# Optimization experiments

Hardware: AMD Instinct MI355X
Metric: run time of the kernel (lower is better)

Reference implementation:

```python
import jax, jax.numpy as jnp
import numpy as np

DIV_COEF = 1.0
EPS = 1e-8  # torch.cosine_similarity default eps


def setup_inputs() -> dict:
    key = jax.random.key(0)
    id_ = jax.random.normal(key, (8192, 512), dtype=jnp.float32)
    return {"id": id_}


def reference(id):
    # cosine similarity via norm + GEMM (math identical to broadcast form)
    norms = jnp.linalg.norm(id, axis=1)                      # [N]
    dots = id @ id.T                                          # [N, N]
    sim = dots / jnp.maximum(norms[:, None] * norms[None, :], EPS)
    n = id.shape[0]
    # zero diagonal, clamp negatives to zero, mean over full NxN
    off_diag = 1.0 - jnp.eye(n, dtype=sim.dtype)
    id_sim = off_diag * sim
    l_id_div = jnp.mean(jnp.where(id_sim < 0, 0.0, id_sim))
    total_loss = DIV_COEF * l_id_div
    return (total_loss, l_id_div)
```

## Files before the change

### kernel.cpp

```cpp
#include <hip/hip_runtime.h>
#include <stdint.h>

#define NROWS 8192
#define KDIM  512
#define BM    256
#define BK    64
#define NKI   (KDIM / BK)
#define NT    (NROWS / BM)
#define NBLK  (NT * (NT + 1) / 2)

typedef __attribute__((ext_vector_type(4)))  int   i32x4;
typedef __attribute__((ext_vector_type(8)))  int   i32x8;
typedef __attribute__((ext_vector_type(16))) float f32x16;

__device__ __forceinline__ void async_copy16(const unsigned char* g, unsigned char* l) {
  __builtin_amdgcn_global_load_lds(
      (const __attribute__((address_space(1))) unsigned int*)g,
      (__attribute__((address_space(3))) unsigned int*)l,
      16, 0, 0);
}

__global__ __launch_bounds__(256) void prep_kernel(
    const float* __restrict__ src, unsigned char* __restrict__ dst,
    float* __restrict__ acc) {
  const int row  = blockIdx.x * 4 + (threadIdx.x >> 6);
  const int lane = threadIdx.x & 63;
  const float4 v0 = ((const float4*)src)[row * 128 + lane * 2];
  const float4 v1 = ((const float4*)src)[row * 128 + lane * 2 + 1];
  float ss = v0.x * v0.x + v0.y * v0.y + v0.z * v0.z + v0.w * v0.w
           + v1.x * v1.x + v1.y * v1.y + v1.z * v1.z + v1.w * v1.w;
  #pragma unroll
  for (int off = 32; off > 0; off >>= 1) ss += __shfl_down(ss, off);
  const float rn = 1.0f / sqrtf(__shfl(ss, 0));
  if (row == 0 && lane == 0) { acc[0] = 0.0f; ((unsigned int*)acc)[1] = 0u; }
  int pk0 = __builtin_amdgcn_cvt_pk_fp8_f32(v0.x * rn, v0.y * rn, 0, false);
  pk0     = __builtin_amdgcn_cvt_pk_fp8_f32(v0.z * rn, v0.w * rn, pk0, true);
  int pk1 = __builtin_amdgcn_cvt_pk_fp8_f32(v1.x * rn, v1.y * rn, 0, false);
  pk1     = __builtin_amdgcn_cvt_pk_fp8_f32(v1.z * rn, v1.w * rn, pk1, true);
  const int cg  = lane >> 1;
  const int win = cg >> 2;
  const int p   = (cg & 3) ^ ((row >> 1) & 3);
  const int hf  = lane & 1;
  uint2 o; o.x = (unsigned int)pk0; o.y = (unsigned int)pk1;
  ((uint2*)dst)[row * 64 + win * 8 + p * 2 + hf] = o;
}

__device__ __forceinline__ int tri_base(int b) {
  return b * NT - (b * (b - 1)) / 2;
}

__global__ __launch_bounds__(512, 2) void sim_reduce_kernel(
    const unsigned char* __restrict__ idn, float* __restrict__ acc,
    float* __restrict__ out) {
  const int idx = blockIdx.x;
  const float Af = 2.0f * NT + 1.0f;
  int bi = (int)((Af - sqrtf(Af * Af - 8.0f * (float)idx)) * 0.5f);
  while (bi > 0 && tri_base(bi) > idx) bi--;
  while (tri_base(bi + 1) <= idx) bi++;
  const int bj = bi + (idx - tri_base(bi));

  __shared__ __align__(16) unsigned char As[2][BM * BK];
  __shared__ __align__(16) unsigned char Bs[2][BM * BK];

  const int tid  = threadIdx.x;
  const int lane = tid & 63;
  const int w    = tid >> 6;
  const int wrow = (w >> 2) * 128;
  const int wcol = (w & 3) * 64;
  const int r32  = lane & 31;
  const int h    = lane >> 5;
  const int rx   = (r32 >> 1) & 3;

  f32x16 acc_f[4][2];
  #pragma unroll
  for (int i = 0; i < 4; i++)
    #pragma unroll
    for (int j = 0; j < 2; j++)
      acc_f[i][j] = (f32x16){0.f, 0.f, 0.f, 0.f, 0.f, 0.f, 0.f, 0.f,
                             0.f, 0.f, 0.f, 0.f, 0.f, 0.f, 0.f, 0.f};

  const unsigned char* gA = idn + (size_t)(bi * BM + (tid >> 2)) * KDIM + (tid & 3) * 16;
  const unsigned char* gB = idn + (size_t)(bj * BM + (tid >> 2)) * KDIM + (tid & 3) * 16;
  const int ldso = tid * 16;

  #pragma unroll
  for (int i = 0; i < 2; i++) async_copy16(gA + (size_t)i * 65536, &As[0][ldso + i * 8192]);
  #pragma unroll
  for (int i = 0; i < 2; i++) async_copy16(gB + (size_t)i * 65536, &Bs[0][ldso + i * 8192]);

  const int p0 = ((2 * h)     ^ rx) * 16;
  const int p1 = ((2 * h + 1) ^ rx) * 16;

  #pragma unroll
  for (int t = 0; t < NKI; ++t) {
    const int cs = t & 1;
    if (t + 1 < NKI) {
      const int ns = cs ^ 1;
      const int ko = (t + 1) * BK;
      #pragma unroll
      for (int i = 0; i < 2; i++)
        async_copy16(gA + ko + (size_t)i * 65536, &As[ns][ldso + i * 8192]);
      #pragma unroll
      for (int i = 0; i < 2; i++)
        async_copy16(gB + ko + (size_t)i * 65536, &Bs[ns][ldso + i * 8192]);
      asm volatile("s_waitcnt vmcnt(4)" ::: "memory");
    } else {
      asm volatile("s_waitcnt vmcnt(0)" ::: "memory");
    }
    asm volatile("s_barrier" ::: "memory");

    i32x8 af[4], bf[2];
    #pragma unroll
    for (int mi = 0; mi < 4; mi++) {
      const unsigned char* ab = &As[cs][(wrow + mi * 32 + r32) * BK];
      const i32x4 alo = *(const i32x4*)(ab + p0);
      const i32x4 ahi = *(const i32x4*)(ab + p1);
      af[mi] = __builtin_shufflevector(alo, ahi, 0, 1, 2, 3, 4, 5, 6, 7);
    }
    #pragma unroll
    for (int ni = 0; ni < 2; ni++) {
      const unsigned char* bb = &Bs[cs][(wcol + ni * 32 + r32) * BK];
      const i32x4 blo = *(const i32x4*)(bb + p0);
      const i32x4 bhi = *(const i32x4*)(bb + p1);
      bf[ni] = __builtin_shufflevector(blo, bhi, 0, 1, 2, 3, 4, 5, 6, 7);
    }
    #pragma unroll
    for (int mi = 0; mi < 4; mi++)
      #pragma unroll
      for (int ni = 0; ni < 2; ni++)
        acc_f[mi][ni] = __builtin_amdgcn_mfma_scale_f32_32x32x64_f8f6f4(
            af[mi], bf[ni], acc_f[mi][ni],
            0, 0,
            0, 0x7F7F7F7Fu,
            0, 0x7F7F7F7Fu);

    asm volatile("s_barrier" ::: "memory");
  }

  float local = 0.f;
  const bool diag = (bi == bj);
  #pragma unroll
  for (int mi = 0; mi < 4; mi++)
    #pragma unroll
    for (int ni = 0; ni < 2; ni++)
      #pragma unroll
      for (int rg = 0; rg < 16; rg++) {
        const int ri = wrow + mi * 32 + (rg & 3) + 8 * (rg >> 2) + 4 * h;
        const int ci = wcol + ni * 32 + r32;
        float v = fmaxf(acc_f[mi][ni][rg], 0.f);
        if (diag && ri == ci) v = 0.f;
        local += v;
      }

  #pragma unroll
  for (int off = 32; off > 0; off >>= 1) local += __shfl_down(local, off);
  __syncthreads();
  float* red = (float*)As;
  if (lane == 0) red[w] = local;
  __syncthreads();
  if (tid == 0) {
    float s = red[0] + red[1] + red[2] + red[3]
            + red[4] + red[5] + red[6] + red[7];
    if (!diag) s *= 2.f;
    atomicAdd(acc, s);
    __threadfence();
    unsigned int done = atomicAdd((unsigned int*)(acc + 1), 1u);
    if (done == NBLK - 1) {
      float total = atomicAdd(acc, 0.0f);
      const float m = total * (1.0f / ((float)NROWS * (float)NROWS));
      out[0] = m;
      out[1] = m;
    }
  }
}

extern "C" void kernel_launch(void* const* d_in, const int* in_sizes, int n_in,
                              void* d_out, int out_size, void* d_ws, size_t ws_size,
                              hipStream_t stream) {
  const float* id = (const float*)d_in[0];
  float* out = (float*)d_out;
  unsigned char* idn = (unsigned char*)d_ws;
  float* acc = (float*)((char*)d_ws + (size_t)NROWS * KDIM);

  prep_kernel<<<NROWS / 4, 256, 0, stream>>>(id, idn, acc);
  sim_reduce_kernel<<<NBLK, 512, 0, stream>>>(idn, acc, out);
}
```

Measured before the change: 96.34 us.

## Split tail triangle tiles into half-height blocks to balance the final wave

The first 512 triangular tiles keep the full 256x256 blocks. The remaining 16 tiles are each split into two 128x256 half blocks, which adds work units for the last partial wave across the CUs. MFMA sections are also wrapped in s_setprio to favour matrix issue. The half blocks reload the B tile, adding some redundant loads, and the runtime MN branch can add overhead or registers in the full path.

Result: slower. 152.8 us (+58.6%).

```diff
diff --git a/kernel.cpp b/kernel.cpp
--- a/kernel.cpp
+++ b/kernel.cpp
@@ -8,6 +8,8 @@
 #define NKI   (KDIM / BK)
 #define NT    (NROWS / BM)
 #define NBLK  (NT * (NT + 1) / 2)
+#define NFULL 512
+#define NGRID (NFULL + 2 * (NBLK - NFULL))
 
 typedef __attribute__((ext_vector_type(4)))  int   i32x4;
 typedef __attribute__((ext_vector_type(8)))  int   i32x8;
@@ -52,7 +54,12 @@
 __global__ __launch_bounds__(512, 2) void sim_reduce_kernel(
     const unsigned char* __restrict__ idn, float* __restrict__ acc,
     float* __restrict__ out) {
-  const int idx = blockIdx.x;
+  const bool fullb = ((int)blockIdx.x < NFULL);
+  const int  idx   = fullb ? (int)blockIdx.x
+                           : NFULL + (((int)blockIdx.x - NFULL) >> 1);
+  const int  half  = fullb ? 0 : (((int)blockIdx.x - NFULL) & 1);
+  const int  MN    = fullb ? 4 : 2;
+
   const float Af = 2.0f * NT + 1.0f;
   int bi = (int)((Af - sqrtf(Af * Af - 8.0f * (float)idx)) * 0.5f);
   while (bi > 0 && tri_base(bi) > idx) bi--;
@@ -65,8 +72,9 @@
   const int tid  = threadIdx.x;
   const int lane = tid & 63;
   const int w    = tid >> 6;
-  const int wrow = (w >> 2) * 128;
-  const int wcol = (w & 3) * 64;
+  const int mrows = fullb ? 128 : 64;
+  const int wrow  = (w >> 2) * mrows;
+  const int wcol  = (w & 3) * 64;
   const int r32  = lane & 31;
   const int h    = lane >> 5;
   const int rx   = (r32 >> 1) & 3;
@@ -79,12 +87,14 @@
       acc_f[i][j] = (f32x16){0.f, 0.f, 0.f, 0.f, 0.f, 0.f, 0.f, 0.f,
                              0.f, 0.f, 0.f, 0.f, 0.f, 0.f, 0.f, 0.f};
 
-  const unsigned char* gA = idn + (size_t)(bi * BM + (tid >> 2)) * KDIM + (tid & 3) * 16;
+  const unsigned char* gA =
+      idn + (size_t)(bi * BM + half * 128 + (tid >> 2)) * KDIM + (tid & 3) * 16;
   const unsigned char* gB = idn + (size_t)(bj * BM + (tid >> 2)) * KDIM + (tid & 3) * 16;
+  const size_t aStride = fullb ? 65536 : 0;
   const int ldso = tid * 16;
 
   #pragma unroll
-  for (int i = 0; i < 2; i++) async_copy16(gA + (size_t)i * 65536, &As[0][ldso + i * 8192]);
+  for (int i = 0; i < 2; i++) async_copy16(gA + (size_t)i * aStride, &As[0][ldso + i * 8192]);
   #pragma unroll
   for (int i = 0; i < 2; i++) async_copy16(gB + (size_t)i * 65536, &Bs[0][ldso + i * 8192]);
 
@@ -99,7 +109,7 @@
       const int ko = (t + 1) * BK;
       #pragma unroll
       for (int i = 0; i < 2; i++)
-        async_copy16(gA + ko + (size_t)i * 65536, &As[ns][ldso + i * 8192]);
+        async_copy16(gA + ko + (size_t)i * aStride, &As[ns][ldso + i * 8192]);
       #pragma unroll
       for (int i = 0; i < 2; i++)
         async_copy16(gB + ko + (size_t)i * 65536, &Bs[ns][ldso + i * 8192]);
@@ -111,13 +121,6 @@
 
     i32x8 af[4], bf[2];
     #pragma unroll
-    for (int mi = 0; mi < 4; mi++) {
-      const unsigned char* ab = &As[cs][(wrow + mi * 32 + r32) * BK];
-      const i32x4 alo = *(const i32x4*)(ab + p0);
-      const i32x4 ahi = *(const i32x4*)(ab + p1);
-      af[mi] = __builtin_shufflevector(alo, ahi, 0, 1, 2, 3, 4, 5, 6, 7);
-    }
-    #pragma unroll
     for (int ni = 0; ni < 2; ni++) {
       const unsigned char* bb = &Bs[cs][(wcol + ni * 32 + r32) * BK];
       const i32x4 blo = *(const i32x4*)(bb + p0);
@@ -126,31 +129,43 @@
     }
     #pragma unroll
     for (int mi = 0; mi < 4; mi++)
+      if (mi < MN) {
+        const unsigned char* ab = &As[cs][(wrow + mi * 32 + r32) * BK];
+        const i32x4 alo = *(const i32x4*)(ab + p0);
+        const i32x4 ahi = *(const i32x4*)(ab + p1);
+        af[mi] = __builtin_shufflevector(alo, ahi, 0, 1, 2, 3, 4, 5, 6, 7);
+      }
+    __builtin_amdgcn_s_setprio(1);
+    #pragma unroll
+    for (int mi = 0; mi < 4; mi++)
+      if (mi < MN)
+        #pragma unroll
+        for (int ni = 0; ni < 2; ni++)
+          acc_f[mi][ni] = __builtin_amdgcn_mfma_scale_f32_32x32x64_f8f6f4(
+              af[mi], bf[ni], acc_f[mi][ni],
+              0, 0,
+              0, 0x7F7F7F7Fu,
+              0, 0x7F7F7F7Fu);
+    __builtin_amdgcn_s_setprio(0);
+
+    asm volatile("s_barrier" ::: "memory");
+  }
+
+  float local = 0.f;
+  const bool diag = (bi == bj);
+  #pragma unroll
+  for (int mi = 0; mi < 4; mi++)
+    if (mi < MN)
       #pragma unroll
       for (int ni = 0; ni < 2; ni++)
-        acc_f[mi][ni] = __builtin_amdgcn_mfma_scale_f32_32x32x64_f8f6f4(
-            af[mi], bf[ni], acc_f[mi][ni],
-            0, 0,
-            0, 0x7F7F7F7Fu,
-            0, 0x7F7F7F7Fu);
-
-    asm volatile("s_barrier" ::: "memory");
-  }
-
-  float local = 0.f;
-  const bool diag = (bi == bj);
-  #pragma unroll
-  for (int mi = 0; mi < 4; mi++)
-    #pragma unroll
-    for (int ni = 0; ni < 2; ni++)
-      #pragma unroll
-      for (int rg = 0; rg < 16; rg++) {
-        const int ri = wrow + mi * 32 + (rg & 3) + 8 * (rg >> 2) + 4 * h;
-        const int ci = wcol + ni * 32 + r32;
-        float v = fmaxf(acc_f[mi][ni][rg], 0.f);
-        if (diag && ri == ci) v = 0.f;
-        local += v;
-      }
+        #pragma unroll
+        for (int rg = 0; rg < 16; rg++) {
+          const int ri = half * 128 + wrow + mi * 32 + (rg & 3) + 8 * (rg >> 2) + 4 * h;
+          const int ci = wcol + ni * 32 + r32;
+          float v = fmaxf(acc_f[mi][ni][rg], 0.f);
+          if (diag && ri == ci) v = 0.f;
+          local += v;
+        }
 
   #pragma unroll
   for (int off = 32; off > 0; off >>= 1) local += __shfl_down(local, off);
@@ -165,7 +180,7 @@
     atomicAdd(acc, s);
     __threadfence();
     unsigned int done = atomicAdd((unsigned int*)(acc + 1), 1u);
-    if (done == NBLK - 1) {
+    if (done == NGRID - 1) {
       float total = atomicAdd(acc, 0.0f);
       const float m = total * (1.0f / ((float)NROWS * (float)NROWS));
       out[0] = m;
@@ -183,5 +198,5 @@
   float* acc = (float*)((char*)d_ws + (size_t)NROWS * KDIM);
 
   prep_kernel<<<NROWS / 4, 256, 0, stream>>>(id, idn, acc);
-  sim_reduce_kernel<<<NBLK, 512, 0, stream>>>(idn, acc, out);
-}
+  sim_reduce_kernel<<<NGRID, 512, 0, stream>>>(idn, acc, out);
+}
```

## Split tail triangular tiles into half-height blocks to balance the wave tail

Applied to the files above, without the earlier changes.

With NT=32 there are 528 triangular 256x256 tiles. The first 512 tiles keep the full 256x256 kernel. The remaining 16 tiles go to a second launch that splits each tile into two 128x256 blocks, giving 32 smaller blocks. The aim is to shorten the final partial wave (tail imbalance) across the CUs. The cost is an extra kernel launch and a lower-reuse tail kernel, and the two launches run serialized on the same stream.

Result: no change. 97.76 us (+1.5%).

```diff
diff --git a/kernel.cpp b/kernel.cpp
--- a/kernel.cpp
+++ b/kernel.cpp
@@ -8,6 +8,9 @@
 #define NKI   (KDIM / BK)
 #define NT    (NROWS / BM)
 #define NBLK  (NT * (NT + 1) / 2)
+#define NFULL 512
+#define NTAIL (NBLK - NFULL)
+#define NTOTAL (NFULL + 2 * NTAIL)
 
 typedef __attribute__((ext_vector_type(4)))  int   i32x4;
 typedef __attribute__((ext_vector_type(8)))  int   i32x8;
@@ -49,44 +52,51 @@
   return b * NT - (b * (b - 1)) / 2;
 }
 
+template <int MN>
 __global__ __launch_bounds__(512, 2) void sim_reduce_kernel(
     const unsigned char* __restrict__ idn, float* __restrict__ acc,
     float* __restrict__ out) {
-  const int idx = blockIdx.x;
+  constexpr int AROWS = MN * 64;
+  constexpr int ACOP  = MN / 2;
+
+  const int idx  = (MN == 4) ? (int)blockIdx.x : NFULL + ((int)blockIdx.x >> 1);
+  const int half = (MN == 4) ? 0 : ((int)blockIdx.x & 1);
+
   const float Af = 2.0f * NT + 1.0f;
   int bi = (int)((Af - sqrtf(Af * Af - 8.0f * (float)idx)) * 0.5f);
   while (bi > 0 && tri_base(bi) > idx) bi--;
   while (tri_base(bi + 1) <= idx) bi++;
   const int bj = bi + (idx - tri_base(bi));
 
-  __shared__ __align__(16) unsigned char As[2][BM * BK];
+  __shared__ __align__(16) unsigned char As[2][AROWS * BK];
   __shared__ __align__(16) unsigned char Bs[2][BM * BK];
 
   const int tid  = threadIdx.x;
   const int lane = tid & 63;
   const int w    = tid >> 6;
-  const int wrow = (w >> 2) * 128;
+  const int wrow = (w >> 2) * (MN * 32);
   const int wcol = (w & 3) * 64;
   const int r32  = lane & 31;
   const int h    = lane >> 5;
   const int rx   = (r32 >> 1) & 3;
 
-  f32x16 acc_f[4][2];
+  f32x16 acc_f[MN][2];
   #pragma unroll
-  for (int i = 0; i < 4; i++)
+  for (int i = 0; i < MN; i++)
     #pragma unroll
     for (int j = 0; j < 2; j++)
       acc_f[i][j] = (f32x16){0.f, 0.f, 0.f, 0.f, 0.f, 0.f, 0.f, 0.f,
                              0.f, 0.f, 0.f, 0.f, 0.f, 0.f, 0.f, 0.f};
 
-  const unsigned char* gA = idn + (size_t)(bi * BM + (tid >> 2)) * KDIM + (tid & 3) * 16;
+  const unsigned char* gA =
+      idn + (size_t)(bi * BM + half * 128 + (tid >> 2)) * KDIM + (tid & 3) * 16;
   const unsigned char* gB = idn + (size_t)(bj * BM + (tid >> 2)) * KDIM + (tid & 3) * 16;
   const int ldso = tid * 16;
 
   #pragma unroll
-  for (int i = 0; i < 2; i++) async_copy16(gA + (size_t)i * 65536, &As[0][ldso + i * 8192]);
+  for (int i = 0; i < ACOP; i++) async_copy16(gA + (size_t)i * 65536, &As[0][ldso + i * 8192]);
   #pragma unroll
-  for (int i = 0; i < 2; i++) async_copy16(gB + (size_t)i * 65536, &Bs[0][ldso + i * 8192]);
+  for (int i = 0; i < 2; i++)    async_copy16(gB + (size_t)i * 65536, &Bs[0][ldso + i * 8192]);
 
   const int p0 = ((2 * h)     ^ rx) * 16;
   const int p1 = ((2 * h + 1) ^ rx) * 16;
@@ -98,25 +108,19 @@
       const int ns = cs ^ 1;
       const int ko = (t + 1) * BK;
       #pragma unroll
-      for (int i = 0; i < 2; i++)
+      for (int i = 0; i < ACOP; i++)
         async_copy16(gA + ko + (size_t)i * 65536, &As[ns][ldso + i * 8192]);
       #pragma unroll
       for (int i = 0; i < 2; i++)
         async_copy16(gB + ko + (size_t)i * 65536, &Bs[ns][ldso + i * 8192]);
-      asm volatile("s_waitcnt vmcnt(4)" ::: "memory");
+      if constexpr (MN == 4) asm volatile("s_waitcnt vmcnt(4)" ::: "memory");
+      else                   asm volatile("s_waitcnt vmcnt(3)" ::: "memory");
     } else {
       asm volatile("s_waitcnt vmcnt(0)" ::: "memory");
     }
     asm volatile("s_barrier" ::: "memory");
 
-    i32x8 af[4], bf[2];
-    #pragma unroll
-    for (int mi = 0; mi < 4; mi++) {
-      const unsigned char* ab = &As[cs][(wrow + mi * 32 + r32) * BK];
-      const i32x4 alo = *(const i32x4*)(ab + p0);
-      const i32x4 ahi = *(const i32x4*)(ab + p1);
-      af[mi] = __builtin_shufflevector(alo, ahi, 0, 1, 2, 3, 4, 5, 6, 7);
-    }
+    i32x8 af[MN], bf[2];
     #pragma unroll
     for (int ni = 0; ni < 2; ni++) {
       const unsigned char* bb = &Bs[cs][(wcol + ni * 32 + r32) * BK];
@@ -125,7 +129,14 @@
       bf[ni] = __builtin_shufflevector(blo, bhi, 0, 1, 2, 3, 4, 5, 6, 7);
     }
     #pragma unroll
-    for (int mi = 0; mi < 4; mi++)
+    for (int mi = 0; mi < MN; mi++) {
+      const unsigned char* ab = &As[cs][(wrow + mi * 32 + r32) * BK];
+      const i32x4 alo = *(const i32x4*)(ab + p0);
+      const i32x4 ahi = *(const i32x4*)(ab + p1);
+      af[mi] = __builtin_shufflevector(alo, ahi, 0, 1, 2, 3, 4, 5, 6, 7);
+    }
+    #pragma unroll
+    for (int mi = 0; mi < MN; mi++)
       #pragma unroll
       for (int ni = 0; ni < 2; ni++)
         acc_f[mi][ni] = __builtin_amdgcn_mfma_scale_f32_32x32x64_f8f6f4(
@@ -140,12 +151,12 @@
   float local = 0.f;
   const bool diag = (bi == bj);
   #pragma unroll
-  for (int mi = 0; mi < 4; mi++)
+  for (int mi = 0; mi < MN; mi++)
     #pragma unroll
     for (int ni = 0; ni < 2; ni++)
       #pragma unroll
       for (int rg = 0; rg < 16; rg++) {
-        const int ri = wrow + mi * 32 + (rg & 3) + 8 * (rg >> 2) + 4 * h;
+        const int ri = half * 128 + wrow + mi * 32 + (rg & 3) + 8 * (rg >> 2) + 4 * h;
         const int ci = wcol + ni * 32 + r32;
         float v = fmaxf(acc_f[mi][ni][rg], 0.f);
         if (diag && ri == ci) v = 0.f;
@@ -155,7 +166,7 @@
   #pragma unroll
   for (int off = 32; off > 0; off >>= 1) local += __shfl_down(local, off);
   __syncthreads();
-  float* red = (float*)As;
+  float* red = (float*)Bs;
   if (lane == 0) red[w] = local;
   __syncthreads();
   if (tid == 0) {
@@ -165,7 +176,7 @@
     atomicAdd(acc, s);
     __threadfence();
     unsigned int done = atomicAdd((unsigned int*)(acc + 1), 1u);
-    if (done == NBLK - 1) {
+    if (done == NTOTAL - 1) {
       float total = atomicAdd(acc, 0.0f);
       const float m = total * (1.0f / ((float)NROWS * (float)NROWS));
       out[0] = m;
@@ -183,5 +194,6 @@
   float* acc = (float*)((char*)d_ws + (size_t)NROWS * KDIM);
 
   prep_kernel<<<NROWS / 4, 256, 0, stream>>>(id, idn, acc);
-  sim_reduce_kernel<<<NBLK, 512, 0, stream>>>(idn, acc, out);
+  sim_reduce_kernel<4><<<NFULL, 512, 0, stream>>>(idn, acc, out);
+  sim_reduce_kernel<2><<<2 * NTAIL, 512, 0, stream>>>(idn, acc, out);
 }
```

## Load MFMA fragments directly from global memory into registers, drop LDS staging

Applied to the files above, without the earlier changes.

Each wave now loads its fp8 A/B fragments straight from global memory (32-byte vector loads) into register double buffers, instead of staging tiles through swizzled LDS with async global_load_lds. The prep kernel writes plain row-major fp8, since the LDS bank swizzle is no longer needed. This removes the LDS traffic and the per-iteration barriers. In exchange, data reuse across waves now relies on L1/L2 instead of shared memory, global traffic per workgroup rises, and register pressure grows.

Result: slower. 137.2 us (+42.4%).

```diff
diff --git a/kernel.cpp b/kernel.cpp
--- a/kernel.cpp
+++ b/kernel.cpp
@@ -9,16 +9,8 @@
 #define NT    (NROWS / BM)
 #define NBLK  (NT * (NT + 1) / 2)
 
-typedef __attribute__((ext_vector_type(4)))  int   i32x4;
 typedef __attribute__((ext_vector_type(8)))  int   i32x8;
 typedef __attribute__((ext_vector_type(16))) float f32x16;
-
-__device__ __forceinline__ void async_copy16(const unsigned char* g, unsigned char* l) {
-  __builtin_amdgcn_global_load_lds(
-      (const __attribute__((address_space(1))) unsigned int*)g,
-      (__attribute__((address_space(3))) unsigned int*)l,
-      16, 0, 0);
-}
 
 __global__ __launch_bounds__(256) void prep_kernel(
     const float* __restrict__ src, unsigned char* __restrict__ dst,
@@ -37,12 +29,8 @@
   pk0     = __builtin_amdgcn_cvt_pk_fp8_f32(v0.z * rn, v0.w * rn, pk0, true);
   int pk1 = __builtin_amdgcn_cvt_pk_fp8_f32(v1.x * rn, v1.y * rn, 0, false);
   pk1     = __builtin_amdgcn_cvt_pk_fp8_f32(v1.z * rn, v1.w * rn, pk1, true);
-  const int cg  = lane >> 1;
-  const int win = cg >> 2;
-  const int p   = (cg & 3) ^ ((row >> 1) & 3);
-  const int hf  = lane & 1;
   uint2 o; o.x = (unsigned int)pk0; o.y = (unsigned int)pk1;
-  ((uint2*)dst)[row * 64 + win * 8 + p * 2 + hf] = o;
+  ((uint2*)dst)[row * 64 + lane] = o;
 }
 
 __device__ __forceinline__ int tri_base(int b) {
@@ -59,8 +47,7 @@
   while (tri_base(bi + 1) <= idx) bi++;
   const int bj = bi + (idx - tri_base(bi));
 
-  __shared__ __align__(16) unsigned char As[2][BM * BK];
-  __shared__ __align__(16) unsigned char Bs[2][BM * BK];
+  __shared__ float red[8];
 
   const int tid  = threadIdx.x;
   const int lane = tid & 63;
@@ -69,7 +56,9 @@
   const int wcol = (w & 3) * 64;
   const int r32  = lane & 31;
   const int h    = lane >> 5;
-  const int rx   = (r32 >> 1) & 3;
+
+  const unsigned char* ga = idn + (size_t)(bi * BM + wrow + r32) * KDIM + h * 32;
+  const unsigned char* gb = idn + (size_t)(bj * BM + wcol + r32) * KDIM + h * 32;
 
   f32x16 acc_f[4][2];
   #pragma unroll
@@ -79,17 +68,14 @@
       acc_f[i][j] = (f32x16){0.f, 0.f, 0.f, 0.f, 0.f, 0.f, 0.f, 0.f,
                              0.f, 0.f, 0.f, 0.f, 0.f, 0.f, 0.f, 0.f};
 
-  const unsigned char* gA = idn + (size_t)(bi * BM + (tid >> 2)) * KDIM + (tid & 3) * 16;
-  const unsigned char* gB = idn + (size_t)(bj * BM + (tid >> 2)) * KDIM + (tid & 3) * 16;
-  const int ldso = tid * 16;
+  i32x8 af[2][4], bf[2][2];
 
   #pragma unroll
-  for (int i = 0; i < 2; i++) async_copy16(gA + (size_t)i * 65536, &As[0][ldso + i * 8192]);
+  for (int mi = 0; mi < 4; mi++)
+    af[0][mi] = *(const i32x8*)(ga + (size_t)mi * 32 * KDIM);
   #pragma unroll
-  for (int i = 0; i < 2; i++) async_copy16(gB + (size_t)i * 65536, &Bs[0][ldso + i * 8192]);
-
-  const int p0 = ((2 * h)     ^ rx) * 16;
-  const int p1 = ((2 * h + 1) ^ rx) * 16;
+  for (int ni = 0; ni < 2; ni++)
+    bf[0][ni] = *(const i32x8*)(gb + (size_t)ni * 32 * KDIM);
 
   #pragma unroll
   for (int t = 0; t < NKI; ++t) {
@@ -98,43 +84,21 @@
       const int ns = cs ^ 1;
       const int ko = (t + 1) * BK;
       #pragma unroll
-      for (int i = 0; i < 2; i++)
-        async_copy16(gA + ko + (size_t)i * 65536, &As[ns][ldso + i * 8192]);
+      for (int mi = 0; mi < 4; mi++)
+        af[ns][mi] = *(const i32x8*)(ga + (size_t)mi * 32 * KDIM + ko);
       #pragma unroll
-      for (int i = 0; i < 2; i++)
-        async_copy16(gB + ko + (size_t)i * 65536, &Bs[ns][ldso + i * 8192]);
-      asm volatile("s_waitcnt vmcnt(4)" ::: "memory");
-    } else {
-      asm volatile("s_waitcnt vmcnt(0)" ::: "memory");
-    }
-    asm volatile("s_barrier" ::: "memory");
-
-    i32x8 af[4], bf[2];
-    #pragma unroll
-    for (int mi = 0; mi < 4; mi++) {
-      const unsigned char* ab = &As[cs][(wrow + mi * 32 + r32) * BK];
-      const i32x4 alo = *(const i32x4*)(ab + p0);
-      const i32x4 ahi = *(const i32x4*)(ab + p1);
-      af[mi] = __builtin_shufflevector(alo, ahi, 0, 1, 2, 3, 4, 5, 6, 7);
-    }
-    #pragma unroll
-    for (int ni = 0; ni < 2; ni++) {
-      const unsigned char* bb = &Bs[cs][(wcol + ni * 32 + r32) * BK];
-      const i32x4 blo = *(const i32x4*)(bb + p0);
-      const i32x4 bhi = *(const i32x4*)(bb + p1);
-      bf[ni] = __builtin_shufflevector(blo, bhi, 0, 1, 2, 3, 4, 5, 6, 7);
+      for (int ni = 0; ni < 2; ni++)
+        bf[ns][ni] = *(const i32x8*)(gb + (size_t)ni * 32 * KDIM + ko);
     }
     #pragma unroll
     for (int mi = 0; mi < 4; mi++)
       #pragma unroll
       for (int ni = 0; ni < 2; ni++)
         acc_f[mi][ni] = __builtin_amdgcn_mfma_scale_f32_32x32x64_f8f6f4(
-            af[mi], bf[ni], acc_f[mi][ni],
+            af[cs][mi], bf[cs][ni], acc_f[mi][ni],
             0, 0,
             0, 0x7F7F7F7Fu,
             0, 0x7F7F7F7Fu);
-
-    asm volatile("s_barrier" ::: "memory");
   }
 
   float local = 0.f;
@@ -154,8 +118,6 @@
 
   #pragma unroll
   for (int off = 32; off > 0; off >>= 1) local += __shfl_down(local, off);
-  __syncthreads();
-  float* red = (float*)As;
   if (lane == 0) red[w] = local;
   __syncthreads();
   if (tid == 0) {
```
